# Optimization experiments

Hardware: AMD Instinct MI355X
Metric: run time of the kernel (lower is better)

Reference implementation:

```python
import jax, jax.numpy as jnp
import numpy as np

B, L, T, H, NL, DFF, DIN = 4096, 64, 256, 8, 4, 1024, 6
HD = T // H
EPS = 1e-9


def setup_inputs() -> dict:
    key = jax.random.key(0)
    ks = jax.random.split(key, 12)
    s = 0.02
    inp = {
        "link_states": jax.random.uniform(ks[0], (B, L, DIN), jnp.float32) * 10.0,
        "link_W1": jax.random.normal(ks[1], (L, DIN, T), jnp.float32) * s,
        "link_b1": jnp.zeros((L, T), jnp.float32),
        "link_W2": jax.random.normal(ks[2], (L, T, T), jnp.float32) * s,
        "link_b2": jnp.zeros((L, T), jnp.float32),
        "Wqkv": jax.random.normal(ks[3], (NL, 3 * T, T), jnp.float32) * s,
        "bqkv": jnp.zeros((NL, 3 * T), jnp.float32),
        "Wo": jax.random.normal(ks[4], (NL, T, T), jnp.float32) * s,
        "bo": jnp.zeros((NL, T), jnp.float32),
        "ln1_g": jnp.ones((NL, T), jnp.float32),
        "ln1_b": jnp.zeros((NL, T), jnp.float32),
        "Wff1": jax.random.normal(ks[5], (NL, DFF, T), jnp.float32) * s,
        "bff1": jnp.zeros((NL, DFF), jnp.float32),
        "Wff2": jax.random.normal(ks[6], (NL, T, DFF), jnp.float32) * s,
        "bff2": jnp.zeros((NL, T), jnp.float32),
        "ln2_g": jnp.ones((NL, T), jnp.float32),
        "ln2_b": jnp.zeros((NL, T), jnp.float32),
        "head_W1": jax.random.normal(ks[7], (T, T), jnp.float32) * s,
        "head_b1": jnp.zeros((T,), jnp.float32),
        "head_W2": jax.random.normal(ks[8], (T, 1), jnp.float32) * s,
        "head_b2": jnp.zeros((1,), jnp.float32),
    }
    return inp


def _layernorm(x, g, b):
    m = x.mean(-1, keepdims=True)
    v = ((x - m) ** 2).mean(-1, keepdims=True)
    return (x - m) * jax.lax.rsqrt(v + 1e-5) * g + b


def _normalize_inputs(x):
    # x: [B, L, 6]
    prop = jnp.clip(x[:, :, 0], 0.0)
    tx = jnp.clip(x[:, :, 1], 0.0)
    sum_pt = prop + tx
    # torch.median returns lower-middle element for even L
    t_ref = jnp.sort(sum_pt, axis=1)[:, (L - 1) // 2][:, None]
    t_ref = jnp.clip(t_ref, 1e-6)
    f0 = prop / t_ref
    f1 = tx / t_ref
    f2 = x[:, :, 2]
    f3 = jnp.log1p(jnp.clip(x[:, :, 3], 0.0))
    f4 = jnp.log1p(jnp.clip(x[:, :, 4], 0.0) / t_ref)
    f5 = jnp.log1p(jnp.clip(x[:, :, 5], 0.0))
    head5 = jnp.stack([f0, f1, f2, f3, f4], axis=-1)  # [B,L,5]
    mean_a = head5.mean(axis=1, keepdims=True)
    std_a = head5.std(axis=1, keepdims=True) + EPS
    head5 = jnp.clip(head5, mean_a - 3.0 * std_a, mean_a + 3.0 * std_a)
    mean = head5.mean(axis=1, keepdims=True)
    std = head5.std(axis=1, keepdims=True) + EPS
    head5 = (head5 - mean) / std
    return jnp.concatenate([head5, f5[:, :, None]], axis=-1)


def _posenc():
    pos = jnp.arange(L, dtype=jnp.float32)[:, None]
    div = jnp.exp(-jnp.log(10000.0) * jnp.arange(0, T, 2, dtype=jnp.float32) / T)
    pe = jnp.zeros((L, T), jnp.float32)
    pe = pe.at[:, 0::2].set(jnp.sin(pos * div))
    pe = pe.at[:, 1::2].set(jnp.cos(pos * div))
    return pe


def _forward(link_states, link_W1, link_b1, link_W2, link_b2, Wqkv, bqkv, Wo, bo,
             ln1_g, ln1_b, Wff1, bff1, Wff2, bff2, ln2_g, ln2_b,
             head_W1, head_b1, head_W2, head_b2):
    x = _normalize_inputs(link_states)  # [B,L,6]
    # per-link (unshared) MLP encoders, batched as grouped matmuls
    h = jax.nn.relu(jnp.einsum('bld,ldt->blt', x, link_W1) + link_b1)
    tok = jnp.einsum('blt,lts->bls', h, link_W2) + link_b2  # [B,L,T]
    y = tok + _posenc()
    scale = 1.0 / np.sqrt(HD)
    for l in range(NL):
        qkv = y @ Wqkv[l].T + bqkv[l]  # [B,L,3T]
        q, k, v = jnp.split(qkv, 3, axis=-1)
        q = q.reshape(B, L, H, HD).transpose(0, 2, 1, 3)
        k = k.reshape(B, L, H, HD).transpose(0, 2, 1, 3)
        v = v.reshape(B, L, H, HD).transpose(0, 2, 1, 3)
        attn = jax.nn.softmax(jnp.einsum('bhqd,bhkd->bhqk', q, k) * scale, axis=-1)
        o = jnp.einsum('bhqk,bhkd->bhqd', attn, v).transpose(0, 2, 1, 3).reshape(B, L, T)
        o = o @ Wo[l].T + bo[l]
        y = _layernorm(y + o, ln1_g[l], ln1_b[l])
        ff = jax.nn.relu(y @ Wff1[l].T + bff1[l]) @ Wff2[l].T + bff2[l]
        y = _layernorm(y + ff, ln2_g[l], ln2_b[l])
    pooled = y.mean(axis=1)  # [B,T]
    hh = jax.nn.relu(pooled @ head_W1 + head_b1)
    values = (hh @ head_W2 + head_b2)[:, 0]  # [B]
    return values


def reference(link_states, link_W1, link_b1, link_W2, link_b2, Wqkv, bqkv, Wo, bo,
              ln1_g, ln1_b, Wff1, bff1, Wff2, bff2, ln2_g, ln2_b,
              head_W1, head_b1, head_W2, head_b2):
    return _forward(link_states, link_W1, link_b1, link_W2, link_b2, Wqkv, bqkv, Wo, bo,
                    ln1_g, ln1_b, Wff1, bff1, Wff2, bff2, ln2_g, ln2_b,
                    head_W1, head_b1, head_W2, head_b2)
```

## Files before the change

kernel.cpp:

```cpp
#include <hip/hip_runtime.h>
#include <cstddef>

#define B_   4096
#define L_   64
#define T_   256
#define H_   8
#define HD_  32
#define NL_  4
#define DFF_ 1024
#define DIN_ 6

typedef unsigned short ushort_t;
typedef __attribute__((ext_vector_type(8))) short bf16x8;
typedef __attribute__((ext_vector_type(4))) float f32x4;

__device__ __forceinline__ float wred_sum(float v) {
#pragma unroll
  for (int off = 32; off >= 1; off >>= 1) v += __shfl_xor(v, off, 64);
  return v;
}
__device__ __forceinline__ ushort_t f2bf(float f) {
  unsigned u = __builtin_bit_cast(unsigned, f);
  u += 0x7fffu + ((u >> 16) & 1u);
  return (ushort_t)(u >> 16);
// ... 172 lines not shown
#pragma unroll
  for (int ni = 0; ni < 4; ++ni) {
    const int cg = wc * 64 + ni * 16 + c_in;
    const float bs = bias[l * 256 + cg] + pe[l * 256 + cg];
#pragma unroll
    for (int mi = 0; mi < 4; ++mi) {
#pragma unroll
      for (int rg = 0; rg < 4; ++rg) {
        const size_t bg = b0 + wr * 64 + mi * 16 + r_in + rg;
        y32[bg * 16384 + l * 256 + cg] = acc[mi][ni][rg] + bs;
      }
    }
  }
}

template <int LAST>
__global__ __launch_bounds__(256, 2) void layer_k(
    float* __restrict__ y32,
    const ushort_t* __restrict__ Wq, const float* __restrict__ bqkv,
    const ushort_t* __restrict__ Wo, const float* __restrict__ bo,
    const float* __restrict__ ln1g, const float* __restrict__ ln1b,
    const ushort_t* __restrict__ Wf1, const float* __restrict__ bf1,
    const ushort_t* __restrict__ Wf2, const float* __restrict__ bf2,
    const float* __restrict__ ln2g, const float* __restrict__ ln2b,
    float* __restrict__ pool) {
  __shared__ ushort_t yF[16384];
  __shared__ ushort_t sc[18432];
  __shared__ float red[4][2][64];
  const int b = blockIdx.x;
  const int tid = threadIdx.x, lane = tid & 63, w = tid >> 6;
  const int li = lane & 15, g = lane >> 4;
  const size_t row0 = (size_t)b * 64;
  const float scale = 0.17677669529663687f;
  ushort_t* bufw = sc + w * 2304;
  ushort_t* vtw  = sc + 9216 + w * 2304;
  ushort_t* zF   = sc;

#pragma unroll
  for (int j = 0; j < 8; ++j) {
    const int u = j * 256 + tid;
    const int row = u & 63, ks = u >> 6;
    const float* src = y32 + (row0 + row) * 256 + ks * 8;
    const float4 a = *(const float4*)src;
    const float4 c = *(const float4*)(src + 4);
    uint4 v;
    v.x = pk2bf(a.x, a.y);
    v.y = pk2bf(a.z, a.w);
    v.z = pk2bf(c.x, c.y);
    v.w = pk2bf(c.z, c.w);
    *(uint4*)&yF[(((row >> 4) * 32 + ks) * 16 + (row & 15)) * 8] = v;
  }
  __syncthreads();

  f32x4 oa2[2][4][2];
#pragma unroll
  for (int hi = 0; hi < 2; ++hi) {
    const int h = w * 2 + hi, hoff = h * 32;

    f32x4 acc[3][2][4];
#pragma unroll
    for (int m = 0; m < 3; ++m)
#pragma unroll
      for (int n = 0; n < 2; ++n)
#pragma unroll
        for (int mi = 0; mi < 4; ++mi) acc[m][n][mi] = (f32x4){0.f, 0.f, 0.f, 0.f};
    __builtin_amdgcn_s_setprio(1);
#pragma unroll
    for (int kt = 0; kt < 8; ++kt) {
      bf16x8 af[4];
#pragma unroll
      for (int mi = 0; mi < 4; ++mi)
        af[mi] = *(const bf16x8*)&yF[((mi * 32 + kt * 4 + g) * 16 + li) * 8];
      bf16x8 bw[3][2];
#pragma unroll
      for (int m = 0; m < 3; ++m)
#pragma unroll
        for (int n = 0; n < 2; ++n)
          bw[m][n] = *(const bf16x8*)(Wq +
              (size_t)(((m * 16 + 2 * h + n) * 32 + kt * 4 + g) * 16 + li) * 8);
#pragma unroll
      for (int m = 0; m < 3; ++m)
#pragma unroll
        for (int n = 0; n < 2; ++n)
#pragma unroll
          for (int mi = 0; mi < 4; ++mi)
            acc[m][n][mi] = __builtin_amdgcn_mfma_f32_16x16x32_bf16(
                af[mi], bw[m][n], acc[m][n][mi], 0, 0, 0);
    }
    __builtin_amdgcn_s_setprio(0);
    float bs[3][2];
#pragma unroll
    for (int m = 0; m < 3; ++m)
#pragma unroll
      for (int n = 0; n < 2; ++n) bs[m][n] = bqkv[m * 256 + hoff + 16 * n + li];

#pragma unroll
    for (int n = 0; n < 2; ++n)
#pragma unroll
      for (int mi = 0; mi < 4; ++mi) {
        const unsigned p0 = pk2bf(acc[0][n][mi][0] + bs[0][n],
                                  acc[0][n][mi][1] + bs[0][n]);
        const unsigned p1 = pk2bf(acc[0][n][mi][2] + bs[0][n],
                                  acc[0][n][mi][3] + bs[0][n]);
        const int base = (16 * mi + 4 * g) * 36 + 16 * n + li;
        bufw[base]       = (ushort_t)p0;
        bufw[base + 36]  = (ushort_t)(p0 >> 16);
        bufw[base + 72]  = (ushort_t)p1;
        bufw[base + 108] = (ushort_t)(p1 >> 16);
      }
    bf16x8 qb[4];
#pragma unroll
    for (int ni = 0; ni < 4; ++ni)
      qb[ni] = *(const bf16x8*)&bufw[(16 * ni + li) * 36 + g * 8];

#pragma unroll
    for (int n = 0; n < 2; ++n)
#pragma unroll
      for (int mi = 0; mi < 4; ++mi) {
        const unsigned p0 = pk2bf(acc[1][n][mi][0] + bs[1][n],
                                  acc[1][n][mi][1] + bs[1][n]);
        const unsigned p1 = pk2bf(acc[1][n][mi][2] + bs[1][n],
                                  acc[1][n][mi][3] + bs[1][n]);
        const int base = (16 * mi + 4 * g) * 36 + 16 * n + li;
        bufw[base]       = (ushort_t)p0;
        bufw[base + 36]  = (ushort_t)(p0 >> 16);
        bufw[base + 72]  = (ushort_t)p1;
        bufw[base + 108] = (ushort_t)(p1 >> 16);
      }
    bf16x8 ka[4];
#pragma unroll
    for (int mi = 0; mi < 4; ++mi)
      ka[mi] = *(const bf16x8*)&bufw[(16 * mi + li) * 36 + g * 8];

#pragma unroll
    for (int n = 0; n < 2; ++n)
#pragma unroll
      for (int mi = 0; mi < 4; ++mi) {
        const unsigned p0 = pk2bf(acc[2][n][mi][0] + bs[2][n],
                                  acc[2][n][mi][1] + bs[2][n]);
        const unsigned p1 = pk2bf(acc[2][n][mi][2] + bs[2][n],
                                  acc[2][n][mi][3] + bs[2][n]);
        *(uint2*)&vtw[(16 * n + li) * 72 + 16 * mi + 4 * g] = make_uint2(p0, p1);
      }
    bf16x8 vb[2][2];
#pragma unroll
    for (int ks = 0; ks < 2; ++ks)
#pragma unroll
      for (int n2 = 0; n2 < 2; ++n2)
        vb[ks][n2] = *(const bf16x8*)&vtw[(16 * n2 + li) * 72 + ks * 32 + g * 8];

#pragma unroll
    for (int mi = 0; mi < 4; ++mi)
#pragma unroll
      for (int n2 = 0; n2 < 2; ++n2) oa2[hi][mi][n2] = (f32x4){0.f, 0.f, 0.f, 0.f};

#pragma unroll
    for (int half = 0; half < 2; ++half) {
      f32x4 s[4][2];
      __builtin_amdgcn_s_setprio(1);
#pragma unroll
      for (int mi = 0; mi < 4; ++mi)
#pragma unroll
        for (int nn = 0; nn < 2; ++nn)
          s[mi][nn] = __builtin_amdgcn_mfma_f32_16x16x32_bf16(
              ka[mi], qb[2 * half + nn], (f32x4){0.f, 0.f, 0.f, 0.f}, 0, 0, 0);
      __builtin_amdgcn_s_setprio(0);

#pragma unroll
      for (int nn = 0; nn < 2; ++nn) {
        float mx = -3.4e38f;
#pragma unroll
        for (int mi = 0; mi < 4; ++mi)
#pragma unroll
          for (int r = 0; r < 4; ++r) {
            s[mi][nn][r] *= scale;
            mx = fmaxf(mx, s[mi][nn][r]);
          }
        mx = fmaxf(mx, __shfl_xor(mx, 16, 64));
        mx = fmaxf(mx, __shfl_xor(mx, 32, 64));
        float sum = 0.f;
#pragma unroll
        for (int mi = 0; mi < 4; ++mi)
#pragma unroll
          for (int r = 0; r < 4; ++r) {
            const float e = expf(s[mi][nn][r] - mx);
            s[mi][nn][r] = e;
            sum += e;
          }
        sum += __shfl_xor(sum, 16, 64);
        sum += __shfl_xor(sum, 32, 64);
        const float inv = 1.f / sum;
        const int qrow = 16 * nn + li;
#pragma unroll
        for (int mi = 0; mi < 4; ++mi) {
          const unsigned lo = pk2bf(s[mi][nn][0] * inv, s[mi][nn][1] * inv);
          const unsigned hi2 = pk2bf(s[mi][nn][2] * inv, s[mi][nn][3] * inv);
          *(uint2*)&bufw[qrow * 72 + 16 * mi + 4 * g] = make_uint2(lo, hi2);
        }
      }

      __builtin_amdgcn_s_setprio(1);
#pragma unroll
      for (int ks = 0; ks < 2; ++ks) {
        bf16x8 pa[2];
#pragma unroll
        for (int m2 = 0; m2 < 2; ++m2)
          pa[m2] = *(const bf16x8*)&bufw[(16 * m2 + li) * 72 + ks * 32 + g * 8];
#pragma unroll
        for (int m2 = 0; m2 < 2; ++m2)
#pragma unroll
          for (int n2 = 0; n2 < 2; ++n2)
            oa2[hi][2 * half + m2][n2] = __builtin_amdgcn_mfma_f32_16x16x32_bf16(
                pa[m2], vb[ks][n2], oa2[hi][2 * half + m2][n2], 0, 0, 0);
      }
      __builtin_amdgcn_s_setprio(0);
    }
  }

  __syncthreads();
#pragma unroll
  for (int hi = 0; hi < 2; ++hi) {
    const int hoff = (2 * w + hi) * 32;
#pragma unroll
    for (int mi = 0; mi < 4; ++mi)
#pragma unroll
      for (int n2 = 0; n2 < 2; ++n2) {
        const unsigned p0 = pk2bf(oa2[hi][mi][n2][0], oa2[hi][mi][n2][1]);
        const unsigned p1 = pk2bf(oa2[hi][mi][n2][2], oa2[hi][mi][n2][3]);
        const int col = hoff + 16 * n2 + li;
        const int base = ((mi * 32 + (col >> 3)) * 16 + 4 * g) * 8 + (col & 7);
        yF[base]      = (ushort_t)p0;
        yF[base + 8]  = (ushort_t)(p0 >> 16);
        yF[base + 16] = (ushort_t)p1;
        yF[base + 24] = (ushort_t)(p1 >> 16);
      }
  }
  __syncthreads();

  f32x4 acc[4][4];
#pragma unroll
  for (int mi = 0; mi < 4; ++mi)
#pragma unroll
    for (int ni = 0; ni < 4; ++ni) acc[mi][ni] = (f32x4){0.f, 0.f, 0.f, 0.f};
  __builtin_amdgcn_s_setprio(1);
#pragma unroll
  for (int kt = 0; kt < 8; ++kt) {
    bf16x8 af[4], bfr[4];
#pragma unroll
    for (int mi = 0; mi < 4; ++mi)
      af[mi] = *(const bf16x8*)&yF[((mi * 32 + kt * 4 + g) * 16 + li) * 8];
#pragma unroll
    for (int ni = 0; ni < 4; ++ni)
      bfr[ni] = *(const bf16x8*)(Wo +
          (size_t)(((4 * w + ni) * 32 + kt * 4 + g) * 16 + li) * 8);
#pragma unroll
    for (int mi = 0; mi < 4; ++mi)
#pragma unroll
      for (int ni = 0; ni < 4; ++ni)
        acc[mi][ni] = __builtin_amdgcn_mfma_f32_16x16x32_bf16(
            af[mi], bfr[ni], acc[mi][ni], 0, 0, 0);
  }
  __builtin_amdgcn_s_setprio(0);

  const int r_in = (lane >> 4) * 4;
  const int c_in = lane & 15;
  float y1r[4][4][4];
#pragma unroll
  for (int mi = 0; mi < 4; ++mi) {
#pragma unroll
    for (int rg = 0; rg < 4; ++rg) {
      const int row_l = 16 * mi + r_in + rg;
      float s1 = 0.f, s2 = 0.f;
#pragma unroll
      for (int ni = 0; ni < 4; ++ni) {
        const int cg = 64 * w + 16 * ni + c_in;
        const float zv = acc[mi][ni][rg] + bo[cg] + y32[(row0 + row_l) * 256 + cg];
        acc[mi][ni][rg] = zv;
        s1 += zv;
        s2 += zv * zv;
      }
#pragma unroll
      for (int off = 1; off <= 8; off <<= 1) {
        s1 += __shfl_xor(s1, off, 64);
        s2 += __shfl_xor(s2, off, 64);
      }
      if (c_in == 0) {
        red[w][0][row_l] = s1;
        red[w][1][row_l] = s2;
      }
    }
  }
  __syncthreads();
#pragma unroll
  for (int mi = 0; mi < 4; ++mi) {
#pragma unroll
    for (int rg = 0; rg < 4; ++rg) {
      const int row_l = 16 * mi + r_in + rg;
      const float S1 = red[0][0][row_l] + red[1][0][row_l] + red[2][0][row_l] + red[3][0][row_l];
      const float S2 = red[0][1][row_l] + red[1][1][row_l] + red[2][1][row_l] + red[3][1][row_l];
      const float m = S1 * (1.f / 256.f);
      const float var = S2 * (1.f / 256.f) - m * m;
      const float rs = rsqrtf(var + 1e-5f);
      float tv[4];
#pragma unroll
      for (int ni = 0; ni < 4; ++ni) {
        const int cg = 64 * w + 16 * ni + c_in;
        tv[ni] = (acc[mi][ni][rg] - m) * rs * ln1g[cg] + ln1b[cg];
        y1r[mi][ni][rg] = tv[ni];
      }
      const unsigned p0 = pk2bf(tv[0], tv[1]);
      const unsigned p1 = pk2bf(tv[2], tv[3]);
#pragma unroll
      for (int ni = 0; ni < 4; ++ni) {
        const int cg = 64 * w + 16 * ni + c_in;
        const unsigned pk = (ni < 2) ? p0 : p1;
        const ushort_t hv = (ni & 1) ? (ushort_t)(pk >> 16) : (ushort_t)pk;
        yF[((mi * 32 + (cg >> 3)) * 16 + (row_l & 15)) * 8 + (cg & 7)] = hv;
      }
    }
  }
  __syncthreads();

  f32x4 acc2[4][4];
#pragma unroll
  for (int mi = 0; mi < 4; ++mi)
#pragma unroll
    for (int ni = 0; ni < 4; ++ni) acc2[mi][ni] = (f32x4){0.f, 0.f, 0.f, 0.f};

#pragma unroll 1
  for (int q = 0; q < 4; ++q) {
#pragma unroll 1
    for (int p = 0; p < 2; ++p) {
      f32x4 acc1[4][2];
#pragma unroll
      for (int mi = 0; mi < 4; ++mi)
#pragma unroll
        for (int n = 0; n < 2; ++n) acc1[mi][n] = (f32x4){0.f, 0.f, 0.f, 0.f};
      __builtin_amdgcn_s_setprio(1);
#pragma unroll
      for (int kt = 0; kt < 8; ++kt) {
        bf16x8 af[4], bw[2];
#pragma unroll
        for (int mi = 0; mi < 4; ++mi)
          af[mi] = *(const bf16x8*)&yF[((mi * 32 + kt * 4 + g) * 16 + li) * 8];
#pragma unroll
        for (int n = 0; n < 2; ++n)
          bw[n] = *(const bf16x8*)(Wf1 +
              (size_t)(((16 * q + 4 * w + 2 * p + n) * 32 + kt * 4 + g) * 16 + li) * 8);
#pragma unroll
        for (int mi = 0; mi < 4; ++mi)
#pragma unroll
          for (int n = 0; n < 2; ++n)
            acc1[mi][n] = __builtin_amdgcn_mfma_f32_16x16x32_bf16(
                af[mi], bw[n], acc1[mi][n], 0, 0, 0);
      }
      __builtin_amdgcn_s_setprio(0);
      if (q && p == 0) __syncthreads();
#pragma unroll
      for (int n = 0; n < 2; ++n) {
        const int kk = 64 * w + 32 * p + 16 * n + li;
        const float bb = bf1[256 * q + kk];
#pragma unroll
        for (int mi = 0; mi < 4; ++mi) {
          const unsigned p0 = pk2bf(fmaxf(acc1[mi][n][0] + bb, 0.f),
                                    fmaxf(acc1[mi][n][1] + bb, 0.f));
          const unsigned p1 = pk2bf(fmaxf(acc1[mi][n][2] + bb, 0.f),
                                    fmaxf(acc1[mi][n][3] + bb, 0.f));
          const int base = ((mi * 32 + (kk >> 3)) * 16 + 4 * g) * 8 + (kk & 7);
          zF[base]      = (ushort_t)p0;
          zF[base + 8]  = (ushort_t)(p0 >> 16);
          zF[base + 16] = (ushort_t)p1;
          zF[base + 24] = (ushort_t)(p1 >> 16);
        }
      }
    }
    __syncthreads();
    __builtin_amdgcn_s_setprio(1);
#pragma unroll
    for (int kt = 0; kt < 8; ++kt) {
      bf16x8 af2[4], bw2[4];
#pragma unroll
      for (int mi = 0; mi < 4; ++mi)
        af2[mi] = *(const bf16x8*)&zF[((mi * 32 + kt * 4 + g) * 16 + li) * 8];
#pragma unroll
      for (int ni = 0; ni < 4; ++ni)
        bw2[ni] = *(const bf16x8*)(Wf2 +
            (size_t)(((4 * w + ni) * 128 + 32 * q + kt * 4 + g) * 16 + li) * 8);
#pragma unroll
      for (int mi = 0; mi < 4; ++mi)
#pragma unroll
        for (int ni = 0; ni < 4; ++ni)
          acc2[mi][ni] = __builtin_amdgcn_mfma_f32_16x16x32_bf16(
              af2[mi], bw2[ni], acc2[mi][ni], 0, 0, 0);
    }
    __builtin_amdgcn_s_setprio(0);
  }

#pragma unroll
  for (int mi = 0; mi < 4; ++mi) {
#pragma unroll
    for (int rg = 0; rg < 4; ++rg) {
      const int row_l = 16 * mi + r_in + rg;
      float s1 = 0.f, s2 = 0.f;
#pragma unroll
      for (int ni = 0; ni < 4; ++ni) {
        const int cg = 64 * w + 16 * ni + c_in;
        const float zv = acc2[mi][ni][rg] + bf2[cg] + y1r[mi][ni][rg];
        acc2[mi][ni][rg] = zv;
        s1 += zv;
        s2 += zv * zv;
      }
#pragma unroll
      for (int off = 1; off <= 8; off <<= 1) {
        s1 += __shfl_xor(s1, off, 64);
        s2 += __shfl_xor(s2, off, 64);
      }
      if (c_in == 0) {
        red[w][0][row_l] = s1;
        red[w][1][row_l] = s2;
      }
    }
  }
  __syncthreads();
  float colsum[4] = {0.f, 0.f, 0.f, 0.f};
#pragma unroll
  for (int mi = 0; mi < 4; ++mi) {
#pragma unroll
    for (int rg = 0; rg < 4; ++rg) {
      const int row_l = 16 * mi + r_in + rg;
      const float S1 = red[0][0][row_l] + red[1][0][row_l] + red[2][0][row_l] + red[3][0][row_l];
      const float S2 = red[0][1][row_l] + red[1][1][row_l] + red[2][1][row_l] + red[3][1][row_l];
      const float m = S1 * (1.f / 256.f);
      const float var = S2 * (1.f / 256.f) - m * m;
      const float rs = rsqrtf(var + 1e-5f);
#pragma unroll
      for (int ni = 0; ni < 4; ++ni) {
        const int cg = 64 * w + 16 * ni + c_in;
        const float v = (acc2[mi][ni][rg] - m) * rs * ln2g[cg] + ln2b[cg];
        if constexpr (LAST) {
          colsum[ni] += v;
        } else {
          y32[(row0 + row_l) * 256 + cg] = v;
        }
      }
    }
  }
  if constexpr (LAST) {
#pragma unroll
    for (int ni = 0; ni < 4; ++ni) {
      float s = colsum[ni];
      s += __shfl_xor(s, 16, 64);
      s += __shfl_xor(s, 32, 64);
      if (g == 0) pool[(size_t)b * 256 + 64 * w + 16 * ni + c_in] = s * (1.f / 64.f);
    }
  }
}

__global__ __launch_bounds__(256) void headgemm_k(
    const float* __restrict__ A, const float* __restrict__ Wt,
    const float* __restrict__ bias, float* __restrict__ out) {
  const int tid = threadIdx.x;
  const int tx = tid & 63, ty = tid >> 6;
  const int cfull = tx * 4;
  const size_t b0 = (size_t)blockIdx.x * 64;

  __shared__ float At[256][68];

  float4 acc[16];
// ... 118 lines not shown
      Wff1, Wff116, 1024 * 256, 5);
  wfrag_k<<<dim3((256 * 1024 + 255) / 256, 1, NL_), 256, 0, stream>>>(
      Wff2, Wff216, 256 * 1024, 7);
  w2t_k<<<(L_ * 256 * 256) / 256, 256, 0, stream>>>(link_W2, W2T16);
  pe_k<<<L_, 128, 0, stream>>>(pe);
  normalize_k<<<B_ / 4, 256, 0, stream>>>(link_states, xn);

  for (int c = 0; c < NC; ++c) {
    const size_t bs = (size_t)c * Bc;

    link1_k<<<(Bc * L_) / 16, 256, 0, stream>>>(xn + bs * L_ * DIN_, link_W1,
                                                link_b1, hbuf);
    linkgemm_k<<<dim3(Bc / 128, 1, L_), 512, 0, stream>>>(
        hbuf, W2T16, link_b2, pe, y32);

    for (int l = 0; l < NL_ - 1; ++l) {
      layer_k<0><<<dim3(Bc, 1, 1), 256, 0, stream>>>(
          y32,
          Wqkv16 + (size_t)l * 768 * 256, bqkv + l * 768,
          Wo16 + (size_t)l * 256 * 256, bo + l * 256,
          ln1_g + l * 256, ln1_b + l * 256,
          Wff116 + (size_t)l * 1024 * 256, bff1 + l * 1024,
          Wff216 + (size_t)l * 256 * 1024, bff2 + l * 256,
          ln2_g + l * 256, ln2_b + l * 256, nullptr);
    }
    {
      const int l = NL_ - 1;
      layer_k<1><<<dim3(Bc, 1, 1), 256, 0, stream>>>(
          y32,
          Wqkv16 + (size_t)l * 768 * 256, bqkv + l * 768,
          Wo16 + (size_t)l * 256 * 256, bo + l * 256,
          ln1_g + l * 256, ln1_b + l * 256,
          Wff116 + (size_t)l * 1024 * 256, bff1 + l * 1024,
          Wff216 + (size_t)l * 256 * 1024, bff2 + l * 256,
          ln2_g + l * 256, ln2_b + l * 256, pooled + bs * T_);
    }
  }

  headgemm_k<<<B_ / 64, 256, 0, stream>>>(pooled, head_W1, head_b1, hh);
  head2_k<<<B_, 64, 0, stream>>>(hh, head_W2, head_b2, (float*)d_out);
}
```

Measured before the change: 3.543 ms.

## Fuse all four transformer layers into one persistent per-sequence kernel

Replaces four per-layer kernel launches with a single kernel that loops over layers and keeps each sequence's activations on chip. The residual stream stays in registers (yres) and the bf16 copy in shared memory between layers, so the fp32 activation buffer is no longer written and re-read from global memory for every layer. This adds register pressure from the persistent residual array and a layer loop, which may lower occupancy or cause spills.

Measured after the change: 5.513 ms. 1.56x slower.

```diff
diff --git a/kernel.cpp b/kernel.cpp
--- a/kernel.cpp
+++ b/kernel.cpp
@@ -210,15 +210,14 @@
   }
 }
 
-template <int LAST>
-__global__ __launch_bounds__(256, 2) void layer_k(
-    float* __restrict__ y32,
-    const ushort_t* __restrict__ Wq, const float* __restrict__ bqkv,
-    const ushort_t* __restrict__ Wo, const float* __restrict__ bo,
-    const float* __restrict__ ln1g, const float* __restrict__ ln1b,
-    const ushort_t* __restrict__ Wf1, const float* __restrict__ bf1,
-    const ushort_t* __restrict__ Wf2, const float* __restrict__ bf2,
-    const float* __restrict__ ln2g, const float* __restrict__ ln2b,
+__global__ __launch_bounds__(256, 2) void layers_k(
+    const float* __restrict__ y32,
+    const ushort_t* __restrict__ Wq0, const float* __restrict__ bqkv0,
+    const ushort_t* __restrict__ Wo0, const float* __restrict__ bo0,
+    const float* __restrict__ ln1g0, const float* __restrict__ ln1b0,
+    const ushort_t* __restrict__ Wf10, const float* __restrict__ bf10,
+    const ushort_t* __restrict__ Wf20, const float* __restrict__ bf20,
+    const float* __restrict__ ln2g0, const float* __restrict__ ln2b0,
     float* __restrict__ pool) {
   __shared__ ushort_t yF[16384];
   __shared__ ushort_t sc[18432];
@@ -232,6 +231,9 @@
   ushort_t* vtw  = sc + 9216 + w * 2304;
   ushort_t* zF   = sc;
 
+  const int r_in = (lane >> 4) * 4;
+  const int c_in = lane & 15;
+
 #pragma unroll
   for (int j = 0; j < 8; ++j) {
     const int u = j * 256 + tid;
@@ -246,408 +248,458 @@
     v.w = pk2bf(c.z, c.w);
     *(uint4*)&yF[(((row >> 4) * 32 + ks) * 16 + (row & 15)) * 8] = v;
   }
+  float yres[4][4][4];
+#pragma unroll
+  for (int mi = 0; mi < 4; ++mi)
+#pragma unroll
+    for (int rg = 0; rg < 4; ++rg) {
+      const int row_l = 16 * mi + r_in + rg;
+#pragma unroll
+      for (int ni = 0; ni < 4; ++ni) {
+        const int cg = 64 * w + 16 * ni + c_in;
+        yres[mi][ni][rg] = y32[(row0 + row_l) * 256 + cg];
+      }
+    }
   __syncthreads();
 
-  f32x4 oa2[2][4][2];
-#pragma unroll
-  for (int hi = 0; hi < 2; ++hi) {
-    const int h = w * 2 + hi, hoff = h * 32;
-
-    f32x4 acc[3][2][4];
-#pragma unroll
-    for (int m = 0; m < 3; ++m)
+#pragma unroll 1
+  for (int l = 0; l < NL_; ++l) {
+    const ushort_t* Wq  = Wq0  + (size_t)l * 768 * 256;
+    const float*    bqkv = bqkv0 + l * 768;
+    const ushort_t* Wo  = Wo0  + (size_t)l * 256 * 256;
+    const float*    bo  = bo0  + l * 256;
+    const float*    ln1g = ln1g0 + l * 256;
+    const float*    ln1b = ln1b0 + l * 256;
+    const ushort_t* Wf1 = Wf10 + (size_t)l * 1024 * 256;
+    const float*    bf1 = bf10 + l * 1024;
+    const ushort_t* Wf2 = Wf20 + (size_t)l * 256 * 1024;
+    const float*    bf2 = bf20 + l * 256;
+    const float*    ln2g = ln2g0 + l * 256;
+    const float*    ln2b = ln2b0 + l * 256;
+
+    f32x4 oa2[2][4][2];
+#pragma unroll
+    for (int hi = 0; hi < 2; ++hi) {
+      const int h = w * 2 + hi, hoff = h * 32;
+
+      f32x4 acc[3][2][4];
+#pragma unroll
+      for (int m = 0; m < 3; ++m)
+#pragma unroll
+        for (int n = 0; n < 2; ++n)
+#pragma unroll
+          for (int mi = 0; mi < 4; ++mi) acc[m][n][mi] = (f32x4){0.f, 0.f, 0.f, 0.f};
+      __builtin_amdgcn_s_setprio(1);
+#pragma unroll
+      for (int kt = 0; kt < 8; ++kt) {
+        bf16x8 af[4];
+#pragma unroll
+        for (int mi = 0; mi < 4; ++mi)
+          af[mi] = *(const bf16x8*)&yF[((mi * 32 + kt * 4 + g) * 16 + li) * 8];
+        bf16x8 bw[3][2];
+#pragma unroll
+        for (int m = 0; m < 3; ++m)
+#pragma unroll
+          for (int n = 0; n < 2; ++n)
+            bw[m][n] = *(const bf16x8*)(Wq +
+                (size_t)(((m * 16 + 2 * h + n) * 32 + kt * 4 + g) * 16 + li) * 8);
+#pragma unroll
+        for (int m = 0; m < 3; ++m)
+#pragma unroll
+          for (int n = 0; n < 2; ++n)
+#pragma unroll
+            for (int mi = 0; mi < 4; ++mi)
+              acc[m][n][mi] = __builtin_amdgcn_mfma_f32_16x16x32_bf16(
+                  af[mi], bw[m][n], acc[m][n][mi], 0, 0, 0);
+      }
+      __builtin_amdgcn_s_setprio(0);
+      float bs[3][2];
+#pragma unroll
+      for (int m = 0; m < 3; ++m)
+#pragma unroll
+        for (int n = 0; n < 2; ++n) bs[m][n] = bqkv[m * 256 + hoff + 16 * n + li];
+
 #pragma unroll
       for (int n = 0; n < 2; ++n)
 #pragma unroll
-        for (int mi = 0; mi < 4; ++mi) acc[m][n][mi] = (f32x4){0.f, 0.f, 0.f, 0.f};
+        for (int mi = 0; mi < 4; ++mi) {
+          const unsigned p0 = pk2bf(acc[0][n][mi][0] + bs[0][n],
+                                    acc[0][n][mi][1] + bs[0][n]);
+          const unsigned p1 = pk2bf(acc[0][n][mi][2] + bs[0][n],
+                                    acc[0][n][mi][3] + bs[0][n]);
+          const int base = (16 * mi + 4 * g) * 36 + 16 * n + li;
+          bufw[base]       = (ushort_t)p0;
+          bufw[base + 36]  = (ushort_t)(p0 >> 16);
+          bufw[base + 72]  = (ushort_t)p1;
+          bufw[base + 108] = (ushort_t)(p1 >> 16);
+        }
+      bf16x8 qb[4];
+#pragma unroll
+      for (int ni = 0; ni < 4; ++ni)
+        qb[ni] = *(const bf16x8*)&bufw[(16 * ni + li) * 36 + g * 8];
+
+#pragma unroll
+      for (int n = 0; n < 2; ++n)
+#pragma unroll
+        for (int mi = 0; mi < 4; ++mi) {
+          const unsigned p0 = pk2bf(acc[1][n][mi][0] + bs[1][n],
+                                    acc[1][n][mi][1] + bs[1][n]);
+          const unsigned p1 = pk2bf(acc[1][n][mi][2] + bs[1][n],
+                                    acc[1][n][mi][3] + bs[1][n]);
+          const int base = (16 * mi + 4 * g) * 36 + 16 * n + li;
+          bufw[base]       = (ushort_t)p0;
+          bufw[base + 36]  = (ushort_t)(p0 >> 16);
+          bufw[base + 72]  = (ushort_t)p1;
+          bufw[base + 108] = (ushort_t)(p1 >> 16);
+        }
+      bf16x8 ka[4];
+#pragma unroll
+      for (int mi = 0; mi < 4; ++mi)
+        ka[mi] = *(const bf16x8*)&bufw[(16 * mi + li) * 36 + g * 8];
+
+#pragma unroll
+      for (int n = 0; n < 2; ++n)
+#pragma unroll
+        for (int mi = 0; mi < 4; ++mi) {
+          const unsigned p0 = pk2bf(acc[2][n][mi][0] + bs[2][n],
+                                    acc[2][n][mi][1] + bs[2][n]);
+          const unsigned p1 = pk2bf(acc[2][n][mi][2] + bs[2][n],
+                                    acc[2][n][mi][3] + bs[2][n]);
+          *(uint2*)&vtw[(16 * n + li) * 72 + 16 * mi + 4 * g] = make_uint2(p0, p1);
+        }
+      bf16x8 vb[2][2];
+#pragma unroll
+      for (int ks = 0; ks < 2; ++ks)
+#pragma unroll
+        for (int n2 = 0; n2 < 2; ++n2)
+          vb[ks][n2] = *(const bf16x8*)&vtw[(16 * n2 + li) * 72 + ks * 32 + g * 8];
+
+#pragma unroll
+      for (int mi = 0; mi < 4; ++mi)
+#pragma unroll
+        for (int n2 = 0; n2 < 2; ++n2) oa2[hi][mi][n2] = (f32x4){0.f, 0.f, 0.f, 0.f};
+
+#pragma unroll
+      for (int half = 0; half < 2; ++half) {
+        f32x4 s[4][2];
+        __builtin_amdgcn_s_setprio(1);
+#pragma unroll
+        for (int mi = 0; mi < 4; ++mi)
+#pragma unroll
+          for (int nn = 0; nn < 2; ++nn)
+            s[mi][nn] = __builtin_amdgcn_mfma_f32_16x16x32_bf16(
+                ka[mi], qb[2 * half + nn], (f32x4){0.f, 0.f, 0.f, 0.f}, 0, 0, 0);
+        __builtin_amdgcn_s_setprio(0);
+
+#pragma unroll
+        for (int nn = 0; nn < 2; ++nn) {
+          float mx = -3.4e38f;
+#pragma unroll
+          for (int mi = 0; mi < 4; ++mi)
+#pragma unroll
+            for (int r = 0; r < 4; ++r) {
+              s[mi][nn][r] *= scale;
+              mx = fmaxf(mx, s[mi][nn][r]);
+            }
+          mx = fmaxf(mx, __shfl_xor(mx, 16, 64));
+          mx = fmaxf(mx, __shfl_xor(mx, 32, 64));
+          float sum = 0.f;
+#pragma unroll
+          for (int mi = 0; mi < 4; ++mi)
+#pragma unroll
+            for (int r = 0; r < 4; ++r) {
+              const float e = expf(s[mi][nn][r] - mx);
+              s[mi][nn][r] = e;
+              sum += e;
+            }
+          sum += __shfl_xor(sum, 16, 64);
+          sum += __shfl_xor(sum, 32, 64);
+          const float inv = 1.f / sum;
+          const int qrow = 16 * nn + li;
+#pragma unroll
+          for (int mi = 0; mi < 4; ++mi) {
+            const unsigned lo = pk2bf(s[mi][nn][0] * inv, s[mi][nn][1] * inv);
+            const unsigned hi2 = pk2bf(s[mi][nn][2] * inv, s[mi][nn][3] * inv);
+            *(uint2*)&bufw[qrow * 72 + 16 * mi + 4 * g] = make_uint2(lo, hi2);
+          }
+        }
+
+        __builtin_amdgcn_s_setprio(1);
+#pragma unroll
+        for (int ks = 0; ks < 2; ++ks) {
+          bf16x8 pa[2];
+#pragma unroll
+          for (int m2 = 0; m2 < 2; ++m2)
+            pa[m2] = *(const bf16x8*)&bufw[(16 * m2 + li) * 72 + ks * 32 + g * 8];
+#pragma unroll
+          for (int m2 = 0; m2 < 2; ++m2)
+#pragma unroll
+            for (int n2 = 0; n2 < 2; ++n2)
+              oa2[hi][2 * half + m2][n2] = __builtin_amdgcn_mfma_f32_16x16x32_bf16(
+                  pa[m2], vb[ks][n2], oa2[hi][2 * half + m2][n2], 0, 0, 0);
+        }
+        __builtin_amdgcn_s_setprio(0);
+      }
+    }
+
+    __syncthreads();
+#pragma unroll
+    for (int hi = 0; hi < 2; ++hi) {
+      const int hoff = (2 * w + hi) * 32;
+#pragma unroll
+      for (int mi = 0; mi < 4; ++mi)
+#pragma unroll
+        for (int n2 = 0; n2 < 2; ++n2) {
+          const unsigned p0 = pk2bf(oa2[hi][mi][n2][0], oa2[hi][mi][n2][1]);
+          const unsigned p1 = pk2bf(oa2[hi][mi][n2][2], oa2[hi][mi][n2][3]);
+          const int col = hoff + 16 * n2 + li;
+          const int base = ((mi * 32 + (col >> 3)) * 16 + 4 * g) * 8 + (col & 7);
+          yF[base]      = (ushort_t)p0;
+          yF[base + 8]  = (ushort_t)(p0 >> 16);
+          yF[base + 16] = (ushort_t)p1;
+          yF[base + 24] = (ushort_t)(p1 >> 16);
+        }
+    }
+    __syncthreads();
+
+    f32x4 acc[4][4];
+#pragma unroll
+    for (int mi = 0; mi < 4; ++mi)
+#pragma unroll
+      for (int ni = 0; ni < 4; ++ni) acc[mi][ni] = (f32x4){0.f, 0.f, 0.f, 0.f};
     __builtin_amdgcn_s_setprio(1);
 #pragma unroll
     for (int kt = 0; kt < 8; ++kt) {
-      bf16x8 af[4];
+      bf16x8 af[4], bfr[4];
 #pragma unroll
       for (int mi = 0; mi < 4; ++mi)
         af[mi] = *(const bf16x8*)&yF[((mi * 32 + kt * 4 + g) * 16 + li) * 8];
-      bf16x8 bw[3][2];
-#pragma unroll
-      for (int m = 0; m < 3; ++m)
-#pragma unroll
-        for (int n = 0; n < 2; ++n)
-          bw[m][n] = *(const bf16x8*)(Wq +
-              (size_t)(((m * 16 + 2 * h + n) * 32 + kt * 4 + g) * 16 + li) * 8);
-#pragma unroll
-      for (int m = 0; m < 3; ++m)
-#pragma unroll
-        for (int n = 0; n < 2; ++n)
+#pragma unroll
+      for (int ni = 0; ni < 4; ++ni)
+        bfr[ni] = *(const bf16x8*)(Wo +
+            (size_t)(((4 * w + ni) * 32 + kt * 4 + g) * 16 + li) * 8);
+#pragma unroll
+      for (int mi = 0; mi < 4; ++mi)
+#pragma unroll
+        for (int ni = 0; ni < 4; ++ni)
+          acc[mi][ni] = __builtin_amdgcn_mfma_f32_16x16x32_bf16(
+              af[mi], bfr[ni], acc[mi][ni], 0, 0, 0);
+    }
+    __builtin_amdgcn_s_setprio(0);
+
+#pragma unroll
+    for (int mi = 0; mi < 4; ++mi) {
+#pragma unroll
+      for (int rg = 0; rg < 4; ++rg) {
+        const int row_l = 16 * mi + r_in + rg;
+        float s1 = 0.f, s2 = 0.f;
+#pragma unroll
+        for (int ni = 0; ni < 4; ++ni) {
+          const int cg = 64 * w + 16 * ni + c_in;
+          const float zv = acc[mi][ni][rg] + bo[cg] + yres[mi][ni][rg];
+          acc[mi][ni][rg] = zv;
+          s1 += zv;
+          s2 += zv * zv;
+        }
+#pragma unroll
+        for (int off = 1; off <= 8; off <<= 1) {
+          s1 += __shfl_xor(s1, off, 64);
+          s2 += __shfl_xor(s2, off, 64);
+        }
+        if (c_in == 0) {
+          red[w][0][row_l] = s1;
+          red[w][1][row_l] = s2;
+        }
+      }
+    }
+    __syncthreads();
+#pragma unroll
+    for (int mi = 0; mi < 4; ++mi) {
+#pragma unroll
+      for (int rg = 0; rg < 4; ++rg) {
+        const int row_l = 16 * mi + r_in + rg;
+        const float S1 = red[0][0][row_l] + red[1][0][row_l] + red[2][0][row_l] + red[3][0][row_l];
+        const float S2 = red[0][1][row_l] + red[1][1][row_l] + red[2][1][row_l] + red[3][1][row_l];
+        const float m = S1 * (1.f / 256.f);
+        const float var = S2 * (1.f / 256.f) - m * m;
+        const float rs = rsqrtf(var + 1e-5f);
+        float tv[4];
+#pragma unroll
+        for (int ni = 0; ni < 4; ++ni) {
+          const int cg = 64 * w + 16 * ni + c_in;
+          tv[ni] = (acc[mi][ni][rg] - m) * rs * ln1g[cg] + ln1b[cg];
+          yres[mi][ni][rg] = tv[ni];
+        }
+        const unsigned p0 = pk2bf(tv[0], tv[1]);
+        const unsigned p1 = pk2bf(tv[2], tv[3]);
+#pragma unroll
+        for (int ni = 0; ni < 4; ++ni) {
+          const int cg = 64 * w + 16 * ni + c_in;
+          const unsigned pk = (ni < 2) ? p0 : p1;
+          const ushort_t hv = (ni & 1) ? (ushort_t)(pk >> 16) : (ushort_t)pk;
+          yF[((mi * 32 + (cg >> 3)) * 16 + (row_l & 15)) * 8 + (cg & 7)] = hv;
+        }
+      }
+    }
+    __syncthreads();
+
+    f32x4 acc2[4][4];
+#pragma unroll
+    for (int mi = 0; mi < 4; ++mi)
+#pragma unroll
+      for (int ni = 0; ni < 4; ++ni) acc2[mi][ni] = (f32x4){0.f, 0.f, 0.f, 0.f};
+
+#pragma unroll 1
+    for (int q = 0; q < 4; ++q) {
+#pragma unroll 1
+      for (int p = 0; p < 2; ++p) {
+        f32x4 acc1[4][2];
+#pragma unroll
+        for (int mi = 0; mi < 4; ++mi)
+#pragma unroll
+          for (int n = 0; n < 2; ++n) acc1[mi][n] = (f32x4){0.f, 0.f, 0.f, 0.f};
+        __builtin_amdgcn_s_setprio(1);
+#pragma unroll
+        for (int kt = 0; kt < 8; ++kt) {
+          bf16x8 af[4], bw[2];
 #pragma unroll
           for (int mi = 0; mi < 4; ++mi)
-            acc[m][n][mi] = __builtin_amdgcn_mfma_f32_16x16x32_bf16(
-                af[mi], bw[m][n], acc[m][n][mi], 0, 0, 0);
-    }
-    __builtin_amdgcn_s_setprio(0);
-    float bs[3][2];
-#pragma unroll
-    for (int m = 0; m < 3; ++m)
-#pragma unroll
-      for (int n = 0; n < 2; ++n) bs[m][n] = bqkv[m * 256 + hoff + 16 * n + li];
-
-#pragma unroll
-    for (int n = 0; n < 2; ++n)
+            af[mi] = *(const bf16x8*)&yF[((mi * 32 + kt * 4 + g) * 16 + li) * 8];
+#pragma unroll
+          for (int n = 0; n < 2; ++n)
+            bw[n] = *(const bf16x8*)(Wf1 +
+                (size_t)(((16 * q + 4 * w + 2 * p + n) * 32 + kt * 4 + g) * 16 + li) * 8);
+#pragma unroll
+          for (int mi = 0; mi < 4; ++mi)
+#pragma unroll
+            for (int n = 0; n < 2; ++n)
+              acc1[mi][n] = __builtin_amdgcn_mfma_f32_16x16x32_bf16(
+                  af[mi], bw[n], acc1[mi][n], 0, 0, 0);
+        }
+        __builtin_amdgcn_s_setprio(0);
+        if (q && p == 0) __syncthreads();
+#pragma unroll
+        for (int n = 0; n < 2; ++n) {
+          const int kk = 64 * w + 32 * p + 16 * n + li;
+          const float bb = bf1[256 * q + kk];
+#pragma unroll
+          for (int mi = 0; mi < 4; ++mi) {
+            const unsigned p0 = pk2bf(fmaxf(acc1[mi][n][0] + bb, 0.f),
+                                      fmaxf(acc1[mi][n][1] + bb, 0.f));
+            const unsigned p1 = pk2bf(fmaxf(acc1[mi][n][2] + bb, 0.f),
+                                      fmaxf(acc1[mi][n][3] + bb, 0.f));
+            const int base = ((mi * 32 + (kk >> 3)) * 16 + 4 * g) * 8 + (kk & 7);
+            zF[base]      = (ushort_t)p0;
+            zF[base + 8]  = (ushort_t)(p0 >> 16);
+            zF[base + 16] = (ushort_t)p1;
+            zF[base + 24] = (ushort_t)(p1 >> 16);
+          }
+        }
+      }
+      __syncthreads();
+      __builtin_amdgcn_s_setprio(1);
+#pragma unroll
+      for (int kt = 0; kt < 8; ++kt) {
+        bf16x8 af2[4], bw2[4];
+#pragma unroll
+        for (int mi = 0; mi < 4; ++mi)
+          af2[mi] = *(const bf16x8*)&zF[((mi * 32 + kt * 4 + g) * 16 + li) * 8];
+#pragma unroll
+        for (int ni = 0; ni < 4; ++ni)
+          bw2[ni] = *(const bf16x8*)(Wf2 +
+              (size_t)(((4 * w + ni) * 128 + 32 * q + kt * 4 + g) * 16 + li) * 8);
+#pragma unroll
+        for (int mi = 0; mi < 4; ++mi)
+#pragma unroll
+          for (int ni = 0; ni < 4; ++ni)
+            acc2[mi][ni] = __builtin_amdgcn_mfma_f32_16x16x32_bf16(
+                af2[mi], bw2[ni], acc2[mi][ni], 0, 0, 0);
+      }
+      __builtin_amdgcn_s_setprio(0);
+    }
+
+#pragma unroll
+    for (int mi = 0; mi < 4; ++mi) {
+#pragma unroll
+      for (int rg = 0; rg < 4; ++rg) {
+        const int row_l = 16 * mi + r_in + rg;
+        float s1 = 0.f, s2 = 0.f;
+#pragma unroll
+        for (int ni = 0; ni < 4; ++ni) {
+          const int cg = 64 * w + 16 * ni + c_in;
+          const float zv = acc2[mi][ni][rg] + bf2[cg] + yres[mi][ni][rg];
+          acc2[mi][ni][rg] = zv;
+          s1 += zv;
+          s2 += zv * zv;
+        }
+#pragma unroll
+        for (int off = 1; off <= 8; off <<= 1) {
+          s1 += __shfl_xor(s1, off, 64);
+          s2 += __shfl_xor(s2, off, 64);
+        }
+        if (c_in == 0) {
+          red[w][0][row_l] = s1;
+          red[w][1][row_l] = s2;
+        }
+      }
+    }
+    __syncthreads();
+    if (l == NL_ - 1) {
+      float colsum[4] = {0.f, 0.f, 0.f, 0.f};
 #pragma unroll
       for (int mi = 0; mi < 4; ++mi) {
-        const unsigned p0 = pk2bf(acc[0][n][mi][0] + bs[0][n],
-                                  acc[0][n][mi][1] + bs[0][n]);
-        const unsigned p1 = pk2bf(acc[0][n][mi][2] + bs[0][n],
-                                  acc[0][n][mi][3] + bs[0][n]);
-        const int base = (16 * mi + 4 * g) * 36 + 16 * n + li;
-        bufw[base]       = (ushort_t)p0;
-        bufw[base + 36]  = (ushort_t)(p0 >> 16);
-        bufw[base + 72]  = (ushort_t)p1;
-        bufw[base + 108] = (ushort_t)(p1 >> 16);
-      }
-    bf16x8 qb[4];
-#pragma unroll
-    for (int ni = 0; ni < 4; ++ni)
-      qb[ni] = *(const bf16x8*)&bufw[(16 * ni + li) * 36 + g * 8];
-
-#pragma unroll
-    for (int n = 0; n < 2; ++n)
+#pragma unroll
+        for (int rg = 0; rg < 4; ++rg) {
+          const int row_l = 16 * mi + r_in + rg;
+          const float S1 = red[0][0][row_l] + red[1][0][row_l] + red[2][0][row_l] + red[3][0][row_l];
+          const float S2 = red[0][1][row_l] + red[1][1][row_l] + red[2][1][row_l] + red[3][1][row_l];
+          const float m = S1 * (1.f / 256.f);
+          const float var = S2 * (1.f / 256.f) - m * m;
+          const float rs = rsqrtf(var + 1e-5f);
+#pragma unroll
+          for (int ni = 0; ni < 4; ++ni) {
+            const int cg = 64 * w + 16 * ni + c_in;
+            colsum[ni] += (acc2[mi][ni][rg] - m) * rs * ln2g[cg] + ln2b[cg];
+          }
+        }
+      }
+#pragma unroll
+      for (int ni = 0; ni < 4; ++ni) {
+        float s = colsum[ni];
+        s += __shfl_xor(s, 16, 64);
+        s += __shfl_xor(s, 32, 64);
+        if (g == 0) pool[(size_t)b * 256 + 64 * w + 16 * ni + c_in] = s * (1.f / 64.f);
+      }
+    } else {
 #pragma unroll
       for (int mi = 0; mi < 4; ++mi) {
-        const unsigned p0 = pk2bf(acc[1][n][mi][0] + bs[1][n],
-                                  acc[1][n][mi][1] + bs[1][n]);
-        const unsigned p1 = pk2bf(acc[1][n][mi][2] + bs[1][n],
-                                  acc[1][n][mi][3] + bs[1][n]);
-        const int base = (16 * mi + 4 * g) * 36 + 16 * n + li;
-        bufw[base]       = (ushort_t)p0;
-        bufw[base + 36]  = (ushort_t)(p0 >> 16);
-        bufw[base + 72]  = (ushort_t)p1;
-        bufw[base + 108] = (ushort_t)(p1 >> 16);
-      }
-    bf16x8 ka[4];
-#pragma unroll
-    for (int mi = 0; mi < 4; ++mi)
-      ka[mi] = *(const bf16x8*)&bufw[(16 * mi + li) * 36 + g * 8];
-
-#pragma unroll
-    for (int n = 0; n < 2; ++n)
-#pragma unroll
-      for (int mi = 0; mi < 4; ++mi) {
-        const unsigned p0 = pk2bf(acc[2][n][mi][0] + bs[2][n],
-                                  acc[2][n][mi][1] + bs[2][n]);
-        const unsigned p1 = pk2bf(acc[2][n][mi][2] + bs[2][n],
-                                  acc[2][n][mi][3] + bs[2][n]);
-        *(uint2*)&vtw[(16 * n + li) * 72 + 16 * mi + 4 * g] = make_uint2(p0, p1);
-      }
-    bf16x8 vb[2][2];
-#pragma unroll
-    for (int ks = 0; ks < 2; ++ks)
-#pragma unroll
-      for (int n2 = 0; n2 < 2; ++n2)
-        vb[ks][n2] = *(const bf16x8*)&vtw[(16 * n2 + li) * 72 + ks * 32 + g * 8];
-
-#pragma unroll
-    for (int mi = 0; mi < 4; ++mi)
-#pragma unroll
-      for (int n2 = 0; n2 < 2; ++n2) oa2[hi][mi][n2] = (f32x4){0.f, 0.f, 0.f, 0.f};
-
-#pragma unroll
-    for (int half = 0; half < 2; ++half) {
-      f32x4 s[4][2];
-      __builtin_amdgcn_s_setprio(1);
-#pragma unroll
-      for (int mi = 0; mi < 4; ++mi)
-#pragma unroll
-        for (int nn = 0; nn < 2; ++nn)
-          s[mi][nn] = __builtin_amdgcn_mfma_f32_16x16x32_bf16(
-              ka[mi], qb[2 * half + nn], (f32x4){0.f, 0.f, 0.f, 0.f}, 0, 0, 0);
-      __builtin_amdgcn_s_setprio(0);
-
-#pragma unroll
-      for (int nn = 0; nn < 2; ++nn) {
-        float mx = -3.4e38f;
-#pragma unroll
-        for (int mi = 0; mi < 4; ++mi)
-#pragma unroll
-          for (int r = 0; r < 4; ++r) {
-            s[mi][nn][r] *= scale;
-            mx = fmaxf(mx, s[mi][nn][r]);
+#pragma unroll
+        for (int rg = 0; rg < 4; ++rg) {
+          const int row_l = 16 * mi + r_in + rg;
+          const float S1 = red[0][0][row_l] + red[1][0][row_l] + red[2][0][row_l] + red[3][0][row_l];
+          const float S2 = red[0][1][row_l] + red[1][1][row_l] + red[2][1][row_l] + red[3][1][row_l];
+          const float m = S1 * (1.f / 256.f);
+          const float var = S2 * (1.f / 256.f) - m * m;
+          const float rs = rsqrtf(var + 1e-5f);
+          float tv[4];
+#pragma unroll
+          for (int ni = 0; ni < 4; ++ni) {
+            const int cg = 64 * w + 16 * ni + c_in;
+            tv[ni] = (acc2[mi][ni][rg] - m) * rs * ln2g[cg] + ln2b[cg];
+            yres[mi][ni][rg] = tv[ni];
           }
-        mx = fmaxf(mx, __shfl_xor(mx, 16, 64));
-        mx = fmaxf(mx, __shfl_xor(mx, 32, 64));
-        float sum = 0.f;
-#pragma unroll
-        for (int mi = 0; mi < 4; ++mi)
-#pragma unroll
-          for (int r = 0; r < 4; ++r) {
-            const float e = expf(s[mi][nn][r] - mx);
-            s[mi][nn][r] = e;
-            sum += e;
+          const unsigned p0 = pk2bf(tv[0], tv[1]);
+          const unsigned p1 = pk2bf(tv[2], tv[3]);
+#pragma unroll
+          for (int ni = 0; ni < 4; ++ni) {
+            const int cg = 64 * w + 16 * ni + c_in;
+            const unsigned pk = (ni < 2) ? p0 : p1;
+            const ushort_t hv = (ni & 1) ? (ushort_t)(pk >> 16) : (ushort_t)pk;
+            yF[((mi * 32 + (cg >> 3)) * 16 + (row_l & 15)) * 8 + (cg & 7)] = hv;
           }
-        sum += __shfl_xor(sum, 16, 64);
-        sum += __shfl_xor(sum, 32, 64);
-        const float inv = 1.f / sum;
-        const int qrow = 16 * nn + li;
-#pragma unroll
-        for (int mi = 0; mi < 4; ++mi) {
-          const unsigned lo = pk2bf(s[mi][nn][0] * inv, s[mi][nn][1] * inv);
-          const unsigned hi2 = pk2bf(s[mi][nn][2] * inv, s[mi][nn][3] * inv);
-          *(uint2*)&bufw[qrow * 72 + 16 * mi + 4 * g] = make_uint2(lo, hi2);
-        }
-      }
-
-      __builtin_amdgcn_s_setprio(1);
-#pragma unroll
-      for (int ks = 0; ks < 2; ++ks) {
-        bf16x8 pa[2];
-#pragma unroll
-        for (int m2 = 0; m2 < 2; ++m2)
-          pa[m2] = *(const bf16x8*)&bufw[(16 * m2 + li) * 72 + ks * 32 + g * 8];
-#pragma unroll
-        for (int m2 = 0; m2 < 2; ++m2)
-#pragma unroll
-          for (int n2 = 0; n2 < 2; ++n2)
-            oa2[hi][2 * half + m2][n2] = __builtin_amdgcn_mfma_f32_16x16x32_bf16(
-                pa[m2], vb[ks][n2], oa2[hi][2 * half + m2][n2], 0, 0, 0);
-      }
-      __builtin_amdgcn_s_setprio(0);
-    }
-  }
-
-  __syncthreads();
-#pragma unroll
-  for (int hi = 0; hi < 2; ++hi) {
-    const int hoff = (2 * w + hi) * 32;
-#pragma unroll
-    for (int mi = 0; mi < 4; ++mi)
-#pragma unroll
-      for (int n2 = 0; n2 < 2; ++n2) {
-        const unsigned p0 = pk2bf(oa2[hi][mi][n2][0], oa2[hi][mi][n2][1]);
-        const unsigned p1 = pk2bf(oa2[hi][mi][n2][2], oa2[hi][mi][n2][3]);
-        const int col = hoff + 16 * n2 + li;
-        const int base = ((mi * 32 + (col >> 3)) * 16 + 4 * g) * 8 + (col & 7);
-        yF[base]      = (ushort_t)p0;
-        yF[base + 8]  = (ushort_t)(p0 >> 16);
-        yF[base + 16] = (ushort_t)p1;
-        yF[base + 24] = (ushort_t)(p1 >> 16);
-      }
-  }
-  __syncthreads();
-
-  f32x4 acc[4][4];
-#pragma unroll
-  for (int mi = 0; mi < 4; ++mi)
-#pragma unroll
-    for (int ni = 0; ni < 4; ++ni) acc[mi][ni] = (f32x4){0.f, 0.f, 0.f, 0.f};
-  __builtin_amdgcn_s_setprio(1);
-#pragma unroll
-  for (int kt = 0; kt < 8; ++kt) {
-    bf16x8 af[4], bfr[4];
-#pragma unroll
-    for (int mi = 0; mi < 4; ++mi)
-      af[mi] = *(const bf16x8*)&yF[((mi * 32 + kt * 4 + g) * 16 + li) * 8];
-#pragma unroll
-    for (int ni = 0; ni < 4; ++ni)
-      bfr[ni] = *(const bf16x8*)(Wo +
-          (size_t)(((4 * w + ni) * 32 + kt * 4 + g) * 16 + li) * 8);
-#pragma unroll
-    for (int mi = 0; mi < 4; ++mi)
-#pragma unroll
-      for (int ni = 0; ni < 4; ++ni)
-        acc[mi][ni] = __builtin_amdgcn_mfma_f32_16x16x32_bf16(
-            af[mi], bfr[ni], acc[mi][ni], 0, 0, 0);
-  }
-  __builtin_amdgcn_s_setprio(0);
-
-  const int r_in = (lane >> 4) * 4;
-  const int c_in = lane & 15;
-  float y1r[4][4][4];
-#pragma unroll
-  for (int mi = 0; mi < 4; ++mi) {
-#pragma unroll
-    for (int rg = 0; rg < 4; ++rg) {
-      const int row_l = 16 * mi + r_in + rg;
-      float s1 = 0.f, s2 = 0.f;
-#pragma unroll
-      for (int ni = 0; ni < 4; ++ni) {
-        const int cg = 64 * w + 16 * ni + c_in;
-        const float zv = acc[mi][ni][rg] + bo[cg] + y32[(row0 + row_l) * 256 + cg];
-        acc[mi][ni][rg] = zv;
-        s1 += zv;
-        s2 += zv * zv;
-      }
-#pragma unroll
-      for (int off = 1; off <= 8; off <<= 1) {
-        s1 += __shfl_xor(s1, off, 64);
-        s2 += __shfl_xor(s2, off, 64);
-      }
-      if (c_in == 0) {
-        red[w][0][row_l] = s1;
-        red[w][1][row_l] = s2;
-      }
-    }
-  }
-  __syncthreads();
-#pragma unroll
-  for (int mi = 0; mi < 4; ++mi) {
-#pragma unroll
-    for (int rg = 0; rg < 4; ++rg) {
-      const int row_l = 16 * mi + r_in + rg;
-      const float S1 = red[0][0][row_l] + red[1][0][row_l] + red[2][0][row_l] + red[3][0][row_l];
-      const float S2 = red[0][1][row_l] + red[1][1][row_l] + red[2][1][row_l] + red[3][1][row_l];
-      const float m = S1 * (1.f / 256.f);
-      const float var = S2 * (1.f / 256.f) - m * m;
-      const float rs = rsqrtf(var + 1e-5f);
-      float tv[4];
-#pragma unroll
-      for (int ni = 0; ni < 4; ++ni) {
-        const int cg = 64 * w + 16 * ni + c_in;
-        tv[ni] = (acc[mi][ni][rg] - m) * rs * ln1g[cg] + ln1b[cg];
-        y1r[mi][ni][rg] = tv[ni];
-      }
-      const unsigned p0 = pk2bf(tv[0], tv[1]);
-      const unsigned p1 = pk2bf(tv[2], tv[3]);
-#pragma unroll
-      for (int ni = 0; ni < 4; ++ni) {
-        const int cg = 64 * w + 16 * ni + c_in;
-        const unsigned pk = (ni < 2) ? p0 : p1;
-        const ushort_t hv = (ni & 1) ? (ushort_t)(pk >> 16) : (ushort_t)pk;
-        yF[((mi * 32 + (cg >> 3)) * 16 + (row_l & 15)) * 8 + (cg & 7)] = hv;
-      }
-    }
-  }
-  __syncthreads();
-
-  f32x4 acc2[4][4];
-#pragma unroll
-  for (int mi = 0; mi < 4; ++mi)
-#pragma unroll
-    for (int ni = 0; ni < 4; ++ni) acc2[mi][ni] = (f32x4){0.f, 0.f, 0.f, 0.f};
-
-#pragma unroll 1
-  for (int q = 0; q < 4; ++q) {
-#pragma unroll 1
-    for (int p = 0; p < 2; ++p) {
-      f32x4 acc1[4][2];
-#pragma unroll
-      for (int mi = 0; mi < 4; ++mi)
-#pragma unroll
-        for (int n = 0; n < 2; ++n) acc1[mi][n] = (f32x4){0.f, 0.f, 0.f, 0.f};
-      __builtin_amdgcn_s_setprio(1);
-#pragma unroll
-      for (int kt = 0; kt < 8; ++kt) {
-        bf16x8 af[4], bw[2];
-#pragma unroll
-        for (int mi = 0; mi < 4; ++mi)
-          af[mi] = *(const bf16x8*)&yF[((mi * 32 + kt * 4 + g) * 16 + li) * 8];
-#pragma unroll
-        for (int n = 0; n < 2; ++n)
-          bw[n] = *(const bf16x8*)(Wf1 +
-              (size_t)(((16 * q + 4 * w + 2 * p + n) * 32 + kt * 4 + g) * 16 + li) * 8);
-#pragma unroll
-        for (int mi = 0; mi < 4; ++mi)
-#pragma unroll
-          for (int n = 0; n < 2; ++n)
-            acc1[mi][n] = __builtin_amdgcn_mfma_f32_16x16x32_bf16(
-                af[mi], bw[n], acc1[mi][n], 0, 0, 0);
-      }
-      __builtin_amdgcn_s_setprio(0);
-      if (q && p == 0) __syncthreads();
-#pragma unroll
-      for (int n = 0; n < 2; ++n) {
-        const int kk = 64 * w + 32 * p + 16 * n + li;
-        const float bb = bf1[256 * q + kk];
-#pragma unroll
-        for (int mi = 0; mi < 4; ++mi) {
-          const unsigned p0 = pk2bf(fmaxf(acc1[mi][n][0] + bb, 0.f),
-                                    fmaxf(acc1[mi][n][1] + bb, 0.f));
-          const unsigned p1 = pk2bf(fmaxf(acc1[mi][n][2] + bb, 0.f),
-                                    fmaxf(acc1[mi][n][3] + bb, 0.f));
-          const int base = ((mi * 32 + (kk >> 3)) * 16 + 4 * g) * 8 + (kk & 7);
-          zF[base]      = (ushort_t)p0;
-          zF[base + 8]  = (ushort_t)(p0 >> 16);
-          zF[base + 16] = (ushort_t)p1;
-          zF[base + 24] = (ushort_t)(p1 >> 16);
-        }
-      }
-    }
-    __syncthreads();
-    __builtin_amdgcn_s_setprio(1);
-#pragma unroll
-    for (int kt = 0; kt < 8; ++kt) {
-      bf16x8 af2[4], bw2[4];
-#pragma unroll
-      for (int mi = 0; mi < 4; ++mi)
-        af2[mi] = *(const bf16x8*)&zF[((mi * 32 + kt * 4 + g) * 16 + li) * 8];
-#pragma unroll
-      for (int ni = 0; ni < 4; ++ni)
-        bw2[ni] = *(const bf16x8*)(Wf2 +
-            (size_t)(((4 * w + ni) * 128 + 32 * q + kt * 4 + g) * 16 + li) * 8);
-#pragma unroll
-      for (int mi = 0; mi < 4; ++mi)
-#pragma unroll
-        for (int ni = 0; ni < 4; ++ni)
-          acc2[mi][ni] = __builtin_amdgcn_mfma_f32_16x16x32_bf16(
-              af2[mi], bw2[ni], acc2[mi][ni], 0, 0, 0);
-    }
-    __builtin_amdgcn_s_setprio(0);
-  }
-
-#pragma unroll
-  for (int mi = 0; mi < 4; ++mi) {
-#pragma unroll
-    for (int rg = 0; rg < 4; ++rg) {
-      const int row_l = 16 * mi + r_in + rg;
-      float s1 = 0.f, s2 = 0.f;
-#pragma unroll
-      for (int ni = 0; ni < 4; ++ni) {
-        const int cg = 64 * w + 16 * ni + c_in;
-        const float zv = acc2[mi][ni][rg] + bf2[cg] + y1r[mi][ni][rg];
-        acc2[mi][ni][rg] = zv;
-        s1 += zv;
-        s2 += zv * zv;
-      }
-#pragma unroll
-      for (int off = 1; off <= 8; off <<= 1) {
-        s1 += __shfl_xor(s1, off, 64);
-        s2 += __shfl_xor(s2, off, 64);
-      }
-      if (c_in == 0) {
-        red[w][0][row_l] = s1;
-        red[w][1][row_l] = s2;
-      }
-    }
-  }
-  __syncthreads();
-  float colsum[4] = {0.f, 0.f, 0.f, 0.f};
-#pragma unroll
-  for (int mi = 0; mi < 4; ++mi) {
-#pragma unroll
-    for (int rg = 0; rg < 4; ++rg) {
-      const int row_l = 16 * mi + r_in + rg;
-      const float S1 = red[0][0][row_l] + red[1][0][row_l] + red[2][0][row_l] + red[3][0][row_l];
-      const float S2 = red[0][1][row_l] + red[1][1][row_l] + red[2][1][row_l] + red[3][1][row_l];
-      const float m = S1 * (1.f / 256.f);
-      const float var = S2 * (1.f / 256.f) - m * m;
-      const float rs = rsqrtf(var + 1e-5f);
-#pragma unroll
-      for (int ni = 0; ni < 4; ++ni) {
-        const int cg = 64 * w + 16 * ni + c_in;
-        const float v = (acc2[mi][ni][rg] - m) * rs * ln2g[cg] + ln2b[cg];
-        if constexpr (LAST) {
-          colsum[ni] += v;
-        } else {
-          y32[(row0 + row_l) * 256 + cg] = v;
-        }
-      }
-    }
-  }
-  if constexpr (LAST) {
-#pragma unroll
-    for (int ni = 0; ni < 4; ++ni) {
-      float s = colsum[ni];
-      s += __shfl_xor(s, 16, 64);
-      s += __shfl_xor(s, 32, 64);
-      if (g == 0) pool[(size_t)b * 256 + 64 * w + 16 * ni + c_in] = s * (1.f / 64.f);
+        }
+      }
+      __syncthreads();
     }
   }
 }
@@ -796,27 +848,11 @@
     linkgemm_k<<<dim3(Bc / 128, 1, L_), 512, 0, stream>>>(
         hbuf, W2T16, link_b2, pe, y32);
 
-    for (int l = 0; l < NL_ - 1; ++l) {
-      layer_k<0><<<dim3(Bc, 1, 1), 256, 0, stream>>>(
-          y32,
-          Wqkv16 + (size_t)l * 768 * 256, bqkv + l * 768,
-          Wo16 + (size_t)l * 256 * 256, bo + l * 256,
-          ln1_g + l * 256, ln1_b + l * 256,
-          Wff116 + (size_t)l * 1024 * 256, bff1 + l * 1024,
-          Wff216 + (size_t)l * 256 * 1024, bff2 + l * 256,
-          ln2_g + l * 256, ln2_b + l * 256, nullptr);
-    }
-    {
-      const int l = NL_ - 1;
-      layer_k<1><<<dim3(Bc, 1, 1), 256, 0, stream>>>(
-          y32,
-          Wqkv16 + (size_t)l * 768 * 256, bqkv + l * 768,
-          Wo16 + (size_t)l * 256 * 256, bo + l * 256,
-          ln1_g + l * 256, ln1_b + l * 256,
-          Wff116 + (size_t)l * 1024 * 256, bff1 + l * 1024,
-          Wff216 + (size_t)l * 256 * 1024, bff2 + l * 256,
-          ln2_g + l * 256, ln2_b + l * 256, pooled + bs * T_);
-    }
+    layers_k<<<dim3(Bc, 1, 1), 256, 0, stream>>>(
+        y32,
+        Wqkv16, bqkv, Wo16, bo, ln1_g, ln1_b,
+        Wff116, bff1, Wff216, bff2, ln2_g, ln2_b,
+        pooled + bs * T_);
   }
 
   headgemm_k<<<B_ / 64, 256, 0, stream>>>(pooled, head_W1, head_b1, hh);
```
